# Kernel optimization log

Hardware: AMD Instinct MI355X
Metric: run time of the kernel (lower is better)

The kernel has to match this reference:

```python
import jax, jax.numpy as jnp
import numpy as np

B, C4, N, L4 = 8, 64, 512, 12
CQ = C4 // 4  # conv output channels


def setup_inputs() -> dict:
    key = jax.random.key(0)
    k_x, k_wc, k_bc, k_wg, k_bg = jax.random.split(key, 5)
    x = jax.random.normal(k_x, (B, C4, N, L4), dtype=jnp.float32)
    # Conv2d(in_dim, in_dim//4, kernel_size=(1,1)) -> pointwise: weight (CQ, C4)
    W_conv = jax.random.normal(k_wc, (CQ, C4), dtype=jnp.float32) / np.sqrt(C4)
    b_conv = jax.random.normal(k_bc, (CQ,), dtype=jnp.float32) * 0.01
    # Linear(in_dim, in_dim)
    W_gcn = jax.random.normal(k_wg, (C4, C4), dtype=jnp.float32) / np.sqrt(C4)
    b_gcn = jax.random.normal(k_bg, (C4,), dtype=jnp.float32) * 0.01
    return {"x": x, "W_conv": W_conv, "b_conv": b_conv, "W_gcn": W_gcn, "b_gcn": b_gcn}


def reference(x, W_conv, b_conv, W_gcn, b_gcn):
    # --- SpatioTemporalCorrelationComputation ---
    # 1x1 conv over channels: (b,c4,n,l) -> (b,cq,n,l)
    Fc = jnp.einsum('oc,bcnl->bonl', W_conv, x) + b_conv[None, :, None, None]
    Fl = Fc[:, :, :, -1]                                   # b,cq,n (last time step)
    xy = jnp.einsum('bcn,bcmt->bnmt', Fl, Fc)              # b,n,n,l4
    xx = jnp.sqrt(jnp.einsum('bcn,bcn->bc', Fl, Fl))       # b,cq
    yy = jnp.sqrt(jnp.einsum('bcnt,bcnt->bc', Fc, Fc))     # b,cq
    l2 = jnp.einsum('bc,bc->b', xx, yy)[:, None, None, None]
    S = xy / l2                                            # b,n,n,l4

    # --- RelationalFeatureExtraction ---
    # Loop-based R[:, :, :, k] = sum_j S[:,k,None,:,j] * F4[:,:,:,j]
    # is exactly this single contraction (Se expansion never materialized):
    R = jnp.einsum('bknj,bcnj->bcnk', S, x)                # b,c4,n,n

    # --- GraphOperation ---
    A = jax.nn.relu(jnp.tanh(jnp.max(R, axis=1)))          # b,n,n
    xg = jnp.einsum('bcnk,bkn->bck', R, A)                 # b,c4,n
    # Linear over channel dim: Fg[b,o,k] = sum_c xg[b,c,k] W[o,c] + bias[o]
    Fg = jnp.einsum('bck,oc->bok', xg, W_gcn) + b_gcn[None, :, None]
    return Fg[..., None]                                   # b,c4,n,1
```

## Files before the change

### kernel.cpp

```cpp
#include <hip/hip_runtime.h>
#include <hip/hip_bf16.h>
#include <math.h>

#define B    8
#define C4   64
#define CQ   16
#define NN   512
#define L4   12
#define KT   128
#define XSP  100

#define O_TH   0
#define O_TL   (O_TH + (size_t)B*1024*NN/2)
#define O_T2H  (O_TL + (size_t)B*1024*NN/2)
#define O_T2L  (O_T2H + (size_t)B*NN*1024/2)
#define O_FL   (O_T2L + (size_t)B*NN*1024/2)
#define O_FLTH (O_FL + (size_t)B*CQ*NN)
#define O_FLTL (O_FLTH + (size_t)B*NN*16/2)
#define O_XX   (O_FLTL + (size_t)B*NN*16/2)
#define O_YY   (O_XX + B*CQ)
#define O_L2   (O_YY + B*CQ)
#define O_AH   (O_L2 + 16)
#define O_AL   (O_AH + (size_t)B*NN*NN/2)
#define O_XG   (O_AL + (size_t)B*NN*NN/2)
#define O_FCG  (O_XG + (size_t)B*C4*NN)

typedef __attribute__((ext_vector_type(8))) short short8;
typedef __attribute__((ext_vector_type(4))) float floatx4;
typedef __attribute__((ext_vector_type(16))) float floatx16;

__device__ inline void split2(float x0, float x1, uint& hw, uint& lw) {
  uint u0 = __float_as_uint(x0), u1 = __float_as_uint(x1);
  uint h0 = u0 >> 16, h1 = u1 >> 16;
  float r0 = x0 - __uint_as_float(h0 << 16);
  float r1 = x1 - __uint_as_float(h1 << 16);
  hw = h0 | (h1 << 16);
  lw = (__float_as_uint(r0) >> 16) | ((__float_as_uint(r1) >> 16) << 16);
}

__global__ __launch_bounds__(256) void k1a_fc(const float* __restrict__ x,
                                              const float* __restrict__ Wc,
                                              const float* __restrict__ bc,
                                              float* __restrict__ ws) {
  int id = blockIdx.x;
  int b = id & 7;
  int nch = id >> 3;
  int n0 = nch * 8;
  int t = threadIdx.x;
  __shared__ __align__(16) float xs[C4*XSP];
  __shared__ float wcs[CQ*65];
  __shared__ float bcs[CQ];
  __shared__ __align__(16) float fcs[8*CQ*L4];

  for (int e = t; e < CQ*C4; e += 256) {
    int q = e >> 6, c = e & 63;
    wcs[q*65 + c] = Wc[e];
  }
  if (t < CQ) bcs[t] = bc[t];
  const float* xb = x + (size_t)b*C4*NN*L4 + (size_t)n0*L4;
  for (int f = t; f < C4*24; f += 256) {
    int c = f / 24, r = f - c*24;
    float4 v = *(const float4*)(xb + (size_t)c*NN*L4 + r*4);
    *(float4*)(xs + c*XSP + r*4) = v;
  }
  __syncthreads();
  {
    int q = t & 15, slot = t >> 4;
    float accv[6];
    #pragma unroll
    for (int i = 0; i < 6; ++i) accv[i] = bcs[q];
    for (int c = 0; c < C4; ++c) {
      float wv = wcs[q*65 + c];
      const float* xc = xs + c*XSP;
      #pragma unroll
      for (int i = 0; i < 6; ++i) accv[i] += wv * xc[slot + 16*i];
    }
    #pragma unroll
    for (int i = 0; i < 6; ++i) {
      int nj = slot + 16*i;
      int nl = nj / L4, j = nj - nl*L4;
      fcs[nl*(CQ*L4) + q*L4 + j] = accv[i];
      if (j == L4-1) ws[O_FL + ((size_t)b*CQ + q)*NN + n0 + nl] = accv[i];
    }
  }
  __syncthreads();
  if (t < CQ) {
    float yy = 0.f, xx = 0.f;
    for (int nl = 0; nl < 8; ++nl) {
      #pragma unroll
      for (int j = 0; j < L4; ++j) { float v = fcs[nl*(CQ*L4) + t*L4 + j]; yy += v*v; }
      float w = fcs[nl*(CQ*L4) + t*L4 + (L4-1)];
      xx += w*w;
    }
    atomicAdd(ws + O_YY + b*CQ + t, yy);
    atomicAdd(ws + O_XX + b*CQ + t, xx);
  }
  float* fcg = ws + O_FCG + (size_t)(b*64 + nch)*1536;
  for (int f = t; f < 384; f += 256)
    *(float4*)(fcg + f*4) = *(const float4*)(fcs + f*4);
}

__global__ __launch_bounds__(256, 4) void k1t_T(const float* __restrict__ x,
                                                float* __restrict__ ws) {
  int id = blockIdx.x;
  int b = id & 7;
  int nch = id >> 3;
  int n0 = nch * 8;
  int t = threadIdx.x;
  __shared__ __align__(16) float xs[C4*XSP];
  __shared__ __align__(16) float fcs[8*CQ*L4];
  const float* xb = x + (size_t)b*C4*NN*L4 + (size_t)n0*L4;
  for (int f = t; f < C4*24; f += 256) {
    int c = f / 24, r = f - c*24;
    float4 v = *(const float4*)(xb + (size_t)c*NN*L4 + r*4);
    *(float4*)(xs + c*XSP + r*4) = v;
  }
  {
    const float* fcg = ws + O_FCG + (size_t)(b*64 + nch)*1536;
    for (int f = t; f < 384; f += 256)
      *(float4*)(fcs + f*4) = *(const float4*)(fcg + f*4);
  }
  __syncthreads();
  int c = t >> 2, q0 = (t & 3) * 4;
  float vals[4][8];
  ushort* T2H = (ushort*)(ws + O_T2H);
  ushort* T2L = (ushort*)(ws + O_T2L);
  for (int nl = 0; nl < 8; ++nl) {
    float xr[L4];
    *(float4*)&xr[0] = *(const float4*)(xs + c*XSP + nl*L4);
    *(float4*)&xr[4] = *(const float4*)(xs + c*XSP + nl*L4 + 4);
    *(float4*)&xr[8] = *(const float4*)(xs + c*XSP + nl*L4 + 8);
    float tvp[4];
    #pragma unroll
    for (int i = 0; i < 4; ++i) {
      const float* fq = fcs + nl*(CQ*L4) + (q0+i)*L4;
      float a = 0.f;
      #pragma unroll
      for (int j = 0; j < L4; ++j) a += fq[j] * xr[j];
      tvp[i] = a;
      vals[i][nl] = a;
    }
    uint hw0, lw0, hw1, lw1;
    split2(tvp[0], tvp[1], hw0, lw0);
    split2(tvp[2], tvp[3], hw1, lw1);
    size_t off2 = ((size_t)b*NN + n0 + nl)*1024 + t*4;
    *(uint2*)(T2H + off2) = make_uint2(hw0, hw1);
    *(uint2*)(T2L + off2) = make_uint2(lw0, lw1);
  }
  ushort* TH = (ushort*)(ws + O_TH);
  ushort* TL = (ushort*)(ws + O_TL);
  #pragma unroll
  for (int i = 0; i < 4; ++i) {
    int m = c*16 + q0 + i;
    uint hw[4], lw[4];
    #pragma unroll
    for (int jj = 0; jj < 4; ++jj)
      split2(vals[i][2*jj], vals[i][2*jj+1], hw[jj], lw[jj]);
    size_t off = ((size_t)b*1024 + m)*NN + n0;
    *(uint4*)(TH + off) = make_uint4(hw[0], hw[1], hw[2], hw[3]);
    *(uint4*)(TL + off) = make_uint4(lw[0], lw[1], lw[2], lw[3]);
  }
}

__global__ __launch_bounds__(256) void k1b_l2flt(float* __restrict__ ws) {
  int t = threadIdx.x;
  if (blockIdx.x == 0) {
    __shared__ float s[B*CQ];
    if (t < B*CQ) s[t] = sqrtf(ws[O_XX + t]) * sqrtf(ws[O_YY + t]);
    __syncthreads();
    if (t < B) {
      float sum = 0.f;
      #pragma unroll
      for (int q = 0; q < CQ; ++q) sum += s[t*CQ + q];
      ws[O_L2 + t] = 1.0f / sum;
    }
  }
  int idx = blockIdx.x*256 + t;
  int b = idx >> 9, k = idx & 511;
  const float* fl = ws + O_FL + (size_t)b*CQ*NN + k;
  ushort h[16], l[16];
  #pragma unroll
  for (int q = 0; q < CQ; ++q) {
    float v = fl[(size_t)q*NN];
    uint u = __float_as_uint(v);
    uint hh = u >> 16;
    float r = v - __uint_as_float(hh << 16);
    h[q] = (ushort)hh;
    l[q] = (ushort)(__float_as_uint(r) >> 16);
  }
  ushort* FH  = (ushort*)(ws + O_FLTH) + (size_t)idx*16;
  ushort* FLo = (ushort*)(ws + O_FLTL) + (size_t)idx*16;
  *(uint4*)(FH)      = *(uint4*)&h[0];
  *(uint4*)(FH + 8)  = *(uint4*)&h[8];
  *(uint4*)(FLo)     = *(uint4*)&l[0];
  *(uint4*)(FLo + 8) = *(uint4*)&l[8];
}

__global__ __launch_bounds__(256, 4) void k2_mfma(float* __restrict__ ws) {
  int id = blockIdx.x;
  int b = id & 7;
  int rest = id >> 3;
  int kh = rest & 1;
  int nch = rest >> 1;
  int t = threadIdx.x;
  int w = t >> 6, lane = t & 63;
  int col = lane & 31, half = lane >> 5;
  float l2inv = ws[O_L2 + b];
  const ushort* FltH = (const ushort*)(ws + O_FLTH);
  const ushort* FltL = (const ushort*)(ws + O_FLTL);
  short8 bhf[2], blf[2];
  int kcol[2];
  #pragma unroll
  for (int kt = 0; kt < 2; ++kt) {
    kcol[kt] = kh*256 + w*64 + kt*32 + col;
    size_t off = ((size_t)(b*NN + kcol[kt]))*16 + half*8;
    bhf[kt] = *(const short8*)(FltH + off);
    blf[kt] = *(const short8*)(FltL + off);
  }
  const ushort* T2H = (const ushort*)(ws + O_T2H) + ((size_t)b*NN + nch*8)*1024;
  const ushort* T2L = (const ushort*)(ws + O_T2L) + ((size_t)b*NN + nch*8)*1024;
  ushort* AH = (ushort*)(ws + O_AH) + ((size_t)b*NN + nch*8)*NN;
  ushort* AL = (ushort*)(ws + O_AL) + ((size_t)b*NN + nch*8)*NN;

  for (int i = 0; i < 8; ++i) {
    short8 ah[2], al[2];
    #pragma unroll
    for (int ct = 0; ct < 2; ++ct) {
      size_t off = (size_t)i*1024 + (ct*32 + col)*16 + half*8;
      ah[ct] = *(const short8*)(T2H + off);
      al[ct] = *(const short8*)(T2L + off);
    }
    floatx16 acc[2][2];
    #pragma unroll
    for (int ct = 0; ct < 2; ++ct)
      #pragma unroll
      for (int kt = 0; kt < 2; ++kt) {
        floatx16 a = {0.f,0.f,0.f,0.f,0.f,0.f,0.f,0.f,
                      0.f,0.f,0.f,0.f,0.f,0.f,0.f,0.f};
        a = __builtin_amdgcn_mfma_f32_32x32x16_bf16(ah[ct], bhf[kt], a, 0, 0, 0);
        a = __builtin_amdgcn_mfma_f32_32x32x16_bf16(ah[ct], blf[kt], a, 0, 0, 0);
        a = __builtin_amdgcn_mfma_f32_32x32x16_bf16(al[ct], bhf[kt], a, 0, 0, 0);
        acc[ct][kt] = a;
      }
    #pragma unroll
    for (int kt = 0; kt < 2; ++kt) {
      float m = acc[0][kt][0];
      #pragma unroll
      for (int ct = 0; ct < 2; ++ct)
        #pragma unroll
        for (int rg = 0; rg < 16; ++rg)
          if (ct + rg) m = fmaxf(m, acc[ct][kt][rg]);
      m = fmaxf(m, __shfl_xor(m, 32));
      float av = fmaxf(tanhf(m*l2inv), 0.f);
      uint u = __float_as_uint(av);
      uint hh = u >> 16;
      float r = av - __uint_as_float(hh << 16);
      ushort lv = (ushort)(__float_as_uint(r) >> 16);
      if (half == 0) {
        AH[(size_t)i*NN + kcol[kt]] = (ushort)hh;
        AL[(size_t)i*NN + kcol[kt]] = lv;
      }
    }
  }
}

__global__ __launch_bounds__(256, 2) void k3_mfma(float* __restrict__ ws) {
  int id = blockIdx.x;
  int b = id & 7;
  int rest = id >> 3;
  int kb = rest & 7;
  int mbb = rest >> 3;
  int t = threadIdx.x;
  int lane = t & 63;
  int w = t >> 6;
  int mw = w >> 1, kw = w & 1;
  int row = lane & 15, quad = lane >> 4;

  __shared__ __align__(16) ushort Ah[128*32];
  __shared__ __align__(16) ushort Al[128*32];
  __shared__ __align__(16) ushort Bh[64*32];
  __shared__ __align__(16) ushort Bl[64*32];

  const ushort* TH = (const ushort*)(ws + O_TH) + ((size_t)b*1024 + mbb*128)*NN;
  const ushort* TL = (const ushort*)(ws + O_TL) + ((size_t)b*1024 + mbb*128)*NN;
  const ushort* AHp = (const ushort*)(ws + O_AH) + ((size_t)b*NN + kb*64)*NN;
  const ushort* ALp = (const ushort*)(ws + O_AL) + ((size_t)b*NN + kb*64)*NN;

  floatx4 acc[4][2];
  #pragma unroll
  for (int i = 0; i < 4; ++i)
    #pragma unroll
    for (int j = 0; j < 2; ++j) acc[i][j] = (floatx4){0.f, 0.f, 0.f, 0.f};

  for (int ksx = 0; ksx < 16; ++ksx) {
    int p0 = ksx*32;
    __syncthreads();
    #pragma unroll
    for (int i = 0; i < 2; ++i) {
      int f = t + 256*i;
      int m = f >> 2, seg = (f & 3) * 8;
      *(uint4*)(Ah + m*32 + seg) = *(const uint4*)(TH + (size_t)m*NN + p0 + seg);
      *(uint4*)(Al + m*32 + seg) = *(const uint4*)(TL + (size_t)m*NN + p0 + seg);
    }
    {
      int j = t >> 2, seg = (t & 3) * 8;
      *(uint4*)(Bh + j*32 + seg) = *(const uint4*)(AHp + (size_t)j*NN + p0 + seg);
      *(uint4*)(Bl + j*32 + seg) = *(const uint4*)(ALp + (size_t)j*NN + p0 + seg);
    }
    __syncthreads();
    short8 bh[2], bl[2];
    #pragma unroll
    for (int kt = 0; kt < 2; ++kt) {
      int jrow = kw*32 + kt*16 + row;
      bh[kt] = *(const short8*)(Bh + jrow*32 + quad*8);
      bl[kt] = *(const short8*)(Bl + jrow*32 + quad*8);
    }
    #pragma unroll
    for (int mt = 0; mt < 4; ++mt) {
      int mrow = mw*64 + mt*16 + row;
      short8 ah = *(const short8*)(Ah + mrow*32 + quad*8);
      short8 al = *(const short8*)(Al + mrow*32 + quad*8);
      #pragma unroll
      for (int kt = 0; kt < 2; ++kt) {
        acc[mt][kt] = __builtin_amdgcn_mfma_f32_16x16x32_bf16(ah, bh[kt], acc[mt][kt], 0, 0, 0);
        acc[mt][kt] = __builtin_amdgcn_mfma_f32_16x16x32_bf16(ah, bl[kt], acc[mt][kt], 0, 0, 0);
        acc[mt][kt] = __builtin_amdgcn_mfma_f32_16x16x32_bf16(al, bh[kt], acc[mt][kt], 0, 0, 0);
      }
    }
  }
  float l2inv = ws[O_L2 + b];
  const float* flb = ws + O_FL + (size_t)b*CQ*NN;
  float fl[2][4];
  #pragma unroll
  for (int kt = 0; kt < 2; ++kt) {
    int kcol = kb*64 + kw*32 + kt*16 + row;
    #pragma unroll
    for (int rg = 0; rg < 4; ++rg)
      fl[kt][rg] = flb[(size_t)(quad*4 + rg)*NN + kcol];
  }
  #pragma unroll
  for (int mt = 0; mt < 4; ++mt) {
    int c = mbb*8 + mw*4 + mt;
    #pragma unroll
    for (int kt = 0; kt < 2; ++kt) {
      float s = fl[kt][0]*acc[mt][kt][0] + fl[kt][1]*acc[mt][kt][1]
              + fl[kt][2]*acc[mt][kt][2] + fl[kt][3]*acc[mt][kt][3];
      s += __shfl_xor(s, 32);
      s += __shfl_xor(s, 16);
      if (quad == 0) {
        int kcol = kb*64 + kw*32 + kt*16 + row;
        ws[O_XG + ((size_t)b*C4 + c)*NN + kcol] = s * l2inv;
      }
    }
  }
}

__global__ __launch_bounds__(256) void k4_out(const float* __restrict__ Wg,
                                              const float* __restrict__ bg,
                                              const float* __restrict__ ws,
                                              float* __restrict__ out) {
  int blk = blockIdx.x;
  int b = blk >> 2, kc = blk & 3;
  int t = threadIdx.x;
  __shared__ float xg[C4][KT+1];
  __shared__ float wg[C4*C4];
  for (int e = t; e < C4*C4; e += 256) wg[e] = Wg[e];
  for (int e = t; e < C4*KT; e += 256) {
    int c = e >> 7, kk = e & (KT-1);
    xg[c][kk] = ws[O_XG + ((size_t)(b*C4 + c))*NN + kc*KT + kk];
  }
  __syncthreads();
  int kk = t & (KT-1);
  int ohalf = t >> 7;
  for (int oi = 0; oi < 32; ++oi) {
    int o = ohalf*32 + oi;
    float acc = bg[o];
    #pragma unroll
    for (int c = 0; c < C4; ++c) acc += wg[o*C4 + c] * xg[c][kk];
    out[((size_t)(b*C4 + o))*NN + kc*KT + kk] = acc;
  }
}

extern "C" void kernel_launch(void* const* d_in, const int* in_sizes, int n_in,
                              void* d_out, int out_size, void* d_ws, size_t ws_size,
                              hipStream_t stream) {
  const float* x  = (const float*)d_in[0];
  const float* Wc = (const float*)d_in[1];
  const float* bc = (const float*)d_in[2];
  const float* Wg = (const float*)d_in[3];
  const float* bg = (const float*)d_in[4];
  float* ws  = (float*)d_ws;
  float* out = (float*)d_out;

  hipMemsetAsync(ws + O_XX, 0, (2*B*CQ + 16)*sizeof(float), stream);

  k1a_fc   <<<B*64,   256, 0, stream>>>(x, Wc, bc, ws);
  k1b_l2flt<<<16,     256, 0, stream>>>(ws);
  k1t_T    <<<B*64,   256, 0, stream>>>(x, ws);
  k2_mfma  <<<B*128,  256, 0, stream>>>(ws);
  k3_mfma  <<<B*64,   256, 0, stream>>>(ws);
  k4_out   <<<B*4,    256, 0, stream>>>(Wg, bg, ws, out);
}
```

Baseline: 154.9 us.

## Fuse conv and transpose kernels, fold l2 and output linear into MFMA kernels

```diff
diff --git a/kernel.cpp b/kernel.cpp
--- a/kernel.cpp
+++ b/kernel.cpp
@@ -7,7 +7,6 @@
 #define CQ   16
 #define NN   512
 #define L4   12
-#define KT   128
 #define XSP  100
 
 #define O_TH   0
@@ -15,15 +14,10 @@
 #define O_T2H  (O_TL + (size_t)B*1024*NN/2)
 #define O_T2L  (O_T2H + (size_t)B*NN*1024/2)
 #define O_FL   (O_T2L + (size_t)B*NN*1024/2)
-#define O_FLTH (O_FL + (size_t)B*CQ*NN)
-#define O_FLTL (O_FLTH + (size_t)B*NN*16/2)
-#define O_XX   (O_FLTL + (size_t)B*NN*16/2)
+#define O_XX   (O_FL + (size_t)B*CQ*NN)
 #define O_YY   (O_XX + B*CQ)
-#define O_L2   (O_YY + B*CQ)
-#define O_AH   (O_L2 + 16)
+#define O_AH   (O_YY + B*CQ)
 #define O_AL   (O_AH + (size_t)B*NN*NN/2)
-#define O_XG   (O_AL + (size_t)B*NN*NN/2)
-#define O_FCG  (O_XG + (size_t)B*C4*NN)
 
 typedef __attribute__((ext_vector_type(8))) short short8;
 typedef __attribute__((ext_vector_type(4))) float floatx4;
@@ -38,10 +32,10 @@
   lw = (__float_as_uint(r0) >> 16) | ((__float_as_uint(r1) >> 16) << 16);
 }
 
-__global__ __launch_bounds__(256) void k1a_fc(const float* __restrict__ x,
-                                              const float* __restrict__ Wc,
-                                              const float* __restrict__ bc,
-                                              float* __restrict__ ws) {
+__global__ __launch_bounds__(256, 4) void k1_fused(const float* __restrict__ x,
+                                                   const float* __restrict__ Wc,
+                                                   const float* __restrict__ bc,
+                                                   float* __restrict__ ws) {
   int id = blockIdx.x;
   int b = id & 7;
   int nch = id >> 3;
@@ -95,32 +89,6 @@
     atomicAdd(ws + O_YY + b*CQ + t, yy);
     atomicAdd(ws + O_XX + b*CQ + t, xx);
   }
-  float* fcg = ws + O_FCG + (size_t)(b*64 + nch)*1536;
-  for (int f = t; f < 384; f += 256)
-    *(float4*)(fcg + f*4) = *(const float4*)(fcs + f*4);
-}
-
-__global__ __launch_bounds__(256, 4) void k1t_T(const float* __restrict__ x,
-                                                float* __restrict__ ws) {
-  int id = blockIdx.x;
-  int b = id & 7;
-  int nch = id >> 3;
-  int n0 = nch * 8;
-  int t = threadIdx.x;
-  __shared__ __align__(16) float xs[C4*XSP];
-  __shared__ __align__(16) float fcs[8*CQ*L4];
-  const float* xb = x + (size_t)b*C4*NN*L4 + (size_t)n0*L4;
-  for (int f = t; f < C4*24; f += 256) {
-    int c = f / 24, r = f - c*24;
-    float4 v = *(const float4*)(xb + (size_t)c*NN*L4 + r*4);
-    *(float4*)(xs + c*XSP + r*4) = v;
-  }
-  {
-    const float* fcg = ws + O_FCG + (size_t)(b*64 + nch)*1536;
-    for (int f = t; f < 384; f += 256)
-      *(float4*)(fcs + f*4) = *(const float4*)(fcg + f*4);
-  }
-  __syncthreads();
   int c = t >> 2, q0 = (t & 3) * 4;
   float vals[4][8];
   ushort* T2H = (ushort*)(ws + O_T2H);
@@ -162,40 +130,6 @@
   }
 }
 
-__global__ __launch_bounds__(256) void k1b_l2flt(float* __restrict__ ws) {
-  int t = threadIdx.x;
-  if (blockIdx.x == 0) {
-    __shared__ float s[B*CQ];
-    if (t < B*CQ) s[t] = sqrtf(ws[O_XX + t]) * sqrtf(ws[O_YY + t]);
-    __syncthreads();
-    if (t < B) {
-      float sum = 0.f;
-      #pragma unroll
-      for (int q = 0; q < CQ; ++q) sum += s[t*CQ + q];
-      ws[O_L2 + t] = 1.0f / sum;
-    }
-  }
-  int idx = blockIdx.x*256 + t;
-  int b = idx >> 9, k = idx & 511;
-  const float* fl = ws + O_FL + (size_t)b*CQ*NN + k;
-  ushort h[16], l[16];
-  #pragma unroll
-  for (int q = 0; q < CQ; ++q) {
-    float v = fl[(size_t)q*NN];
-    uint u = __float_as_uint(v);
-    uint hh = u >> 16;
-    float r = v - __uint_as_float(hh << 16);
-    h[q] = (ushort)hh;
-    l[q] = (ushort)(__float_as_uint(r) >> 16);
-  }
-  ushort* FH  = (ushort*)(ws + O_FLTH) + (size_t)idx*16;
-  ushort* FLo = (ushort*)(ws + O_FLTL) + (size_t)idx*16;
-  *(uint4*)(FH)      = *(uint4*)&h[0];
-  *(uint4*)(FH + 8)  = *(uint4*)&h[8];
-  *(uint4*)(FLo)     = *(uint4*)&l[0];
-  *(uint4*)(FLo + 8) = *(uint4*)&l[8];
-}
-
 __global__ __launch_bounds__(256, 4) void k2_mfma(float* __restrict__ ws) {
   int id = blockIdx.x;
   int b = id & 7;
@@ -205,17 +139,31 @@
   int t = threadIdx.x;
   int w = t >> 6, lane = t & 63;
   int col = lane & 31, half = lane >> 5;
-  float l2inv = ws[O_L2 + b];
-  const ushort* FltH = (const ushort*)(ws + O_FLTH);
-  const ushort* FltL = (const ushort*)(ws + O_FLTL);
+
+  __shared__ float l2tmp[CQ];
+  if (t < CQ) l2tmp[t] = sqrtf(ws[O_XX + b*CQ + t]) * sqrtf(ws[O_YY + b*CQ + t]);
+  __syncthreads();
+  float l2sum = 0.f;
+  #pragma unroll
+  for (int q = 0; q < CQ; ++q) l2sum += l2tmp[q];
+  float l2inv = 1.0f / l2sum;
+
+  const float* flb = ws + O_FL + (size_t)b*CQ*NN;
   short8 bhf[2], blf[2];
   int kcol[2];
   #pragma unroll
   for (int kt = 0; kt < 2; ++kt) {
     kcol[kt] = kh*256 + w*64 + kt*32 + col;
-    size_t off = ((size_t)(b*NN + kcol[kt]))*16 + half*8;
-    bhf[kt] = *(const short8*)(FltH + off);
-    blf[kt] = *(const short8*)(FltL + off);
+    float f[8];
+    #pragma unroll
+    for (int e = 0; e < 8; ++e) f[e] = flb[(size_t)(half*8 + e)*NN + kcol[kt]];
+    #pragma unroll
+    for (int p = 0; p < 4; ++p) {
+      uint hw, lw;
+      split2(f[2*p], f[2*p+1], hw, lw);
+      ((uint*)&bhf[kt])[p] = hw;
+      ((uint*)&blf[kt])[p] = lw;
+    }
   }
   const ushort* T2H = (const ushort*)(ws + O_T2H) + ((size_t)b*NN + nch*8)*1024;
   const ushort* T2L = (const ushort*)(ws + O_T2L) + ((size_t)b*NN + nch*8)*1024;
@@ -251,7 +199,8 @@
         for (int rg = 0; rg < 16; ++rg)
           if (ct + rg) m = fmaxf(m, acc[ct][kt][rg]);
       m = fmaxf(m, __shfl_xor(m, 32));
-      float av = fmaxf(tanhf(m*l2inv), 0.f);
+      float xp = fmaxf(m * l2inv, 0.f);
+      float av = 1.f - __fdividef(2.f, __expf(2.f * xp) + 1.f);
       uint u = __float_as_uint(av);
       uint hh = u >> 16;
       float r = av - __uint_as_float(hh << 16);
@@ -264,7 +213,10 @@
   }
 }
 
-__global__ __launch_bounds__(256, 2) void k3_mfma(float* __restrict__ ws) {
+__global__ __launch_bounds__(256, 2) void k3_mfma(const float* __restrict__ Wg,
+                                                  const float* __restrict__ bg,
+                                                  float* __restrict__ ws,
+                                                  float* __restrict__ out) {
   int id = blockIdx.x;
   int b = id & 7;
   int rest = id >> 3;
@@ -280,6 +232,15 @@
   __shared__ __align__(16) ushort Al[128*32];
   __shared__ __align__(16) ushort Bh[64*32];
   __shared__ __align__(16) ushort Bl[64*32];
+  __shared__ float l2tmp[CQ];
+  __shared__ float wgs[C4*8];
+  __shared__ float xg_s[8][64];
+
+  if (t < CQ) l2tmp[t] = sqrtf(ws[O_XX + b*CQ + t]) * sqrtf(ws[O_YY + b*CQ + t]);
+  for (int e = t; e < C4*8; e += 256) {
+    int o = e >> 3, cl = e & 7;
+    wgs[e] = Wg[o*C4 + mbb*8 + cl];
+  }
 
   const ushort* TH = (const ushort*)(ws + O_TH) + ((size_t)b*1024 + mbb*128)*NN;
   const ushort* TL = (const ushort*)(ws + O_TL) + ((size_t)b*1024 + mbb*128)*NN;
@@ -328,7 +289,11 @@
       }
     }
   }
-  float l2inv = ws[O_L2 + b];
+  float l2sum = 0.f;
+  #pragma unroll
+  for (int q = 0; q < CQ; ++q) l2sum += l2tmp[q];
+  float l2inv = 1.0f / l2sum;
+
   const float* flb = ws + O_FL + (size_t)b*CQ*NN;
   float fl[2][4];
   #pragma unroll
@@ -340,44 +305,26 @@
   }
   #pragma unroll
   for (int mt = 0; mt < 4; ++mt) {
-    int c = mbb*8 + mw*4 + mt;
     #pragma unroll
     for (int kt = 0; kt < 2; ++kt) {
       float s = fl[kt][0]*acc[mt][kt][0] + fl[kt][1]*acc[mt][kt][1]
               + fl[kt][2]*acc[mt][kt][2] + fl[kt][3]*acc[mt][kt][3];
       s += __shfl_xor(s, 32);
       s += __shfl_xor(s, 16);
-      if (quad == 0) {
-        int kcol = kb*64 + kw*32 + kt*16 + row;
-        ws[O_XG + ((size_t)b*C4 + c)*NN + kcol] = s * l2inv;
-      }
-    }
-  }
-}
-
-__global__ __launch_bounds__(256) void k4_out(const float* __restrict__ Wg,
-                                              const float* __restrict__ bg,
-                                              const float* __restrict__ ws,
-                                              float* __restrict__ out) {
-  int blk = blockIdx.x;
-  int b = blk >> 2, kc = blk & 3;
-  int t = threadIdx.x;
-  __shared__ float xg[C4][KT+1];
-  __shared__ float wg[C4*C4];
-  for (int e = t; e < C4*C4; e += 256) wg[e] = Wg[e];
-  for (int e = t; e < C4*KT; e += 256) {
-    int c = e >> 7, kk = e & (KT-1);
-    xg[c][kk] = ws[O_XG + ((size_t)(b*C4 + c))*NN + kc*KT + kk];
+      if (quad == 0)
+        xg_s[mw*4 + mt][kw*32 + kt*16 + row] = s * l2inv;
+    }
   }
   __syncthreads();
-  int kk = t & (KT-1);
-  int ohalf = t >> 7;
-  for (int oi = 0; oi < 32; ++oi) {
-    int o = ohalf*32 + oi;
-    float acc = bg[o];
-    #pragma unroll
-    for (int c = 0; c < C4; ++c) acc += wg[o*C4 + c] * xg[c][kk];
-    out[((size_t)(b*C4 + o))*NN + kc*KT + kk] = acc;
+  int kl = t & 63, og = t >> 6;
+  #pragma unroll
+  for (int oi = 0; oi < 16; ++oi) {
+    int o = og*16 + oi;
+    float a = 0.f;
+    #pragma unroll
+    for (int cl = 0; cl < 8; ++cl) a += wgs[o*8 + cl] * xg_s[cl][kl];
+    if (mbb == 0) a += bg[o];
+    atomicAdd(out + ((size_t)(b*C4 + o))*NN + kb*64 + kl, a);
   }
 }
 
@@ -392,12 +339,10 @@
   float* ws  = (float*)d_ws;
   float* out = (float*)d_out;
 
-  hipMemsetAsync(ws + O_XX, 0, (2*B*CQ + 16)*sizeof(float), stream);
-
-  k1a_fc   <<<B*64,   256, 0, stream>>>(x, Wc, bc, ws);
-  k1b_l2flt<<<16,     256, 0, stream>>>(ws);
-  k1t_T    <<<B*64,   256, 0, stream>>>(x, ws);
-  k2_mfma  <<<B*128,  256, 0, stream>>>(ws);
-  k3_mfma  <<<B*64,   256, 0, stream>>>(ws);
-  k4_out   <<<B*4,    256, 0, stream>>>(Wg, bg, ws, out);
-}
+  hipMemsetAsync(ws + O_XX, 0, 2*B*CQ*sizeof(float), stream);
+  hipMemsetAsync(out, 0, (size_t)out_size, stream);
+
+  k1_fused<<<B*64,  256, 0, stream>>>(x, Wc, bc, ws);
+  k2_mfma <<<B*128, 256, 0, stream>>>(ws);
+  k3_mfma <<<B*64,  256, 0, stream>>>(Wg, bg, ws, out);
+}
```

Result: slower. 238.2 us (+53.8%).
